# Optimization experiments

Hardware: AMD Instinct MI355X
Metric: run time of the kernel (lower is better)

Reference implementation:

```python
import jax, jax.numpy as jnp
import numpy as np

N, E, FDIM, HID, HEADS, C, L, G = 50000, 800000, 512, 256, 8, 32, 3, 64
EPS = 1e-5


def setup_inputs() -> dict:
    key = jax.random.key(0)
    ks = jax.random.split(key, 16)
    x = jax.random.normal(ks[0], (N, FDIM), dtype=jnp.float32)
    edge_index = jax.random.randint(ks[1], (2, E), 0, N, dtype=jnp.int32)
    batch = jnp.sort(jax.random.randint(ks[2], (N,), 0, G, dtype=jnp.int32))
    s = lambda f: 1.0 / np.sqrt(f)
    return {
        "x": x,
        "edge_index": edge_index,
        "batch": batch,
        "in_w": jax.random.normal(ks[3], (FDIM, HID), jnp.float32) * s(FDIM),
        "in_b": jnp.zeros((HID,), jnp.float32),
        "gat_w": jax.random.normal(ks[4], (L, HID, HID), jnp.float32) * s(HID),
        "att_src": jax.random.normal(ks[5], (L, HEADS, C), jnp.float32) * s(C),
        "att_dst": jax.random.normal(ks[6], (L, HEADS, C), jnp.float32) * s(C),
        "gat_b": jnp.zeros((L, HID), jnp.float32),
        "res_w": jax.random.normal(ks[7], (L, HID, HID), jnp.float32) * s(HID),
        "res_b": jnp.zeros((L, HID), jnp.float32),
        "ln_g": jnp.ones((L, HID), jnp.float32),
        "ln_b": jnp.zeros((L, HID), jnp.float32),
        "pool_w": jax.random.normal(ks[8], (2 * HID, HID), jnp.float32) * s(2 * HID),
        "pool_b": jnp.zeros((HID,), jnp.float32),
    }


def _gat_layer(h, src, dst, w, a_src, a_dst, b):
    # PyG GATConv, concat=True, negative_slope=0.2, dropout inactive (eval)
    xh = (h @ w).reshape(N, HEADS, C)                      # [N,H,C]
    asn = jnp.einsum('nhc,hc->nh', xh, a_src)              # [N,H]
    adn = jnp.einsum('nhc,hc->nh', xh, a_dst)
    e = jax.nn.leaky_relu(asn[src] + adn[dst], 0.2)        # [E2,H]
    # scatter-softmax over destination neighborhoods
    m = jax.ops.segment_max(e, dst, num_segments=N)
    m = jnp.where(jnp.isfinite(m), m, 0.0)
    ex = jnp.exp(e - m[dst])
    den = jax.ops.segment_sum(ex, dst, num_segments=N)
    alpha = ex / (den[dst] + 1e-16)                        # [E2,H]
    msg = xh[src] * alpha[:, :, None]                      # [E2,H,C]
    out = jax.ops.segment_sum(msg, dst, num_segments=N)    # [N,H,C]
    return out.reshape(N, HID) + b


def _layer_norm(h, g, b):
    mu = jnp.mean(h, axis=-1, keepdims=True)
    var = jnp.mean((h - mu) ** 2, axis=-1, keepdims=True)
    return (h - mu) * jax.lax.rsqrt(var + EPS) * g + b


def reference(x, edge_index, batch, in_w, in_b, gat_w, att_src, att_dst, gat_b,
              res_w, res_b, ln_g, ln_b, pool_w, pool_b):
    loops = jnp.arange(N, dtype=edge_index.dtype)          # GATConv add_self_loops=True
    src = jnp.concatenate([edge_index[0], loops])
    dst = jnp.concatenate([edge_index[1], loops])
    h = x @ in_w + in_b
    for i in range(L):
        h_res = h @ res_w[i] + res_b[i]
        h = _gat_layer(h, src, dst, gat_w[i], att_src[i], att_dst[i], gat_b[i])
        h = jax.nn.relu(_layer_norm(h + h_res, ln_g[i], ln_b[i]))
    ones = jnp.ones((N,), h.dtype)
    cnt = jax.ops.segment_sum(ones, batch, num_segments=G)
    h_mean = jax.ops.segment_sum(h, batch, num_segments=G) / jnp.maximum(cnt, 1.0)[:, None]
    h_max = jax.ops.segment_max(h, batch, num_segments=G)
    h_cat = jnp.concatenate([h_mean, h_max], axis=1)       # [G, 2*HID]
    return jax.nn.relu(h_cat @ pool_w + pool_b)            # [G, HID]
```

## Files before the change

kernel.cpp:

```cpp
#include <hip/hip_runtime.h>
#include <math.h>

#define N_NODES 50000
#define E_EDGES 800000
#define E2 (E_EDGES + N_NODES)
#define M_PAD 50048
#define FDIM 512
#define HID 256
#define HEADS 8
#define CDIM 32
#define LAYERS 3
#define GRAPHS 64
#define LN_EPS 1e-5f
#define POOL_P 16

typedef unsigned short ushort_t;
typedef __attribute__((ext_vector_type(8))) short short8v;
typedef __attribute__((ext_vector_type(4))) float f32x4;

__device__ __forceinline__ float bf2f(ushort_t u) {
    union { unsigned int i; float f; } v;
    v.i = ((unsigned int)u) << 16;
    return v.f;
}
__device__ __forceinline__ ushort_t f2bf(float f) {
    union { float f; unsigned int u; } v;
    v.f = f;
    unsigned int r = (v.u + 0x7FFFu + ((v.u >> 16) & 1u)) >> 16;
    return (ushort_t)r;
}
__device__ __forceinline__ void gload_lds16(const void* g, void* l) {
    __builtin_amdgcn_global_load_lds(
        (const __attribute__((address_space(1))) void*)g,
        (__attribute__((address_space(3))) void*)l, 16, 0, 0);
}

__global__ void k_count(const int* __restrict__ ei, int* __restrict__ cnt) {
    int e = blockIdx.x * 256 + threadIdx.x;
    if (e >= E2) return;
    int dst = (e < E_EDGES) ? ei[E_EDGES + e] : (e - E_EDGES);
    atomicAdd(&cnt[dst], 1);
}

__global__ void k_scan1(const int* __restrict__ cnt, int* __restrict__ part) {
    __shared__ int s[256];
    int t = threadIdx.x;
    int i = blockIdx.x * 256 + t;
    s[t] = (i < N_NODES) ? cnt[i] : 0;
    __syncthreads();
    for (int d = 128; d > 0; d >>= 1) {
        if (t < d) s[t] += s[t + d];
        __syncthreads();
    }
    if (t == 0) part[blockIdx.x] = s[0];
}

__global__ void k_scan2(int* __restrict__ part, int nb, int* __restrict__ rowptr) {
    __shared__ int s[256];
    int t = threadIdx.x;
    int v = (t < nb) ? part[t] : 0;
    s[t] = v;
    __syncthreads();
    for (int d = 1; d < 256; d <<= 1) {
        int x = (t >= d) ? s[t - d] : 0;
        __syncthreads();
        s[t] += x;
        __syncthreads();
    }
    if (t < nb) part[t] = s[t] - v;
    if (t == 255) rowptr[N_NODES] = s[255];
}

__global__ void k_scan3(const int* __restrict__ cnt, const int* __restrict__ part,
                        int* __restrict__ rowptr) {
    __shared__ int s[256];
    int t = threadIdx.x;
    int i = blockIdx.x * 256 + t;
    int v = (i < N_NODES) ? cnt[i] : 0;
    s[t] = v;
    __syncthreads();
    for (int d = 1; d < 256; d <<= 1) {
        int x = (t >= d) ? s[t - d] : 0;
        __syncthreads();
        s[t] += x;
        __syncthreads();
    }
    if (i < N_NODES) rowptr[i] = part[blockIdx.x] + s[t] - v;
}

__global__ void k_fill(const int* __restrict__ ei, const int* __restrict__ rowptr,
                       int* __restrict__ fill, int* __restrict__ colv) {
    int e = blockIdx.x * 256 + threadIdx.x;
    if (e >= E2) return;
    int src, dst;
    if (e < E_EDGES) { src = ei[e]; dst = ei[E_EDGES + e]; }
    else             { src = dst = e - E_EDGES; }
    int pos = atomicAdd(&fill[dst], 1);
    colv[rowptr[dst] + pos] = src;
}

__global__ void k_bounds(const int* __restrict__ batch, int* __restrict__ rowstart) {
    int n = blockIdx.x * 256 + threadIdx.x;
    if (n >= N_NODES) return;
    int b = batch[n];
    int bp = (n == 0) ? -1 : batch[n - 1];
    for (int g = bp + 1; g <= b; ++g) rowstart[g] = n;
    if (n == N_NODES - 1) {
        for (int g = b + 1; g <= GRAPHS; ++g) rowstart[g] = N_NODES;
    }
}

__global__ __launch_bounds__(256) void k_cast_x(const float* __restrict__ x,
                                                ushort_t* __restrict__ xb) {
    long long i8 = ((long long)blockIdx.x * 256 + threadIdx.x) * 8;
    if (i8 >= (long long)M_PAD * FDIM) return;
    int row = (int)(i8 >> 9);
    ushort_t o[8];
    if (row < N_NODES) {
        const float* p = x + i8;
        #pragma unroll
        for (int j = 0; j < 8; ++j) o[j] = f2bf(p[j]);
    } else {
        #pragma unroll
        for (int j = 0; j < 8; ++j) o[j] = 0;
    }
    *(short8v*)(xb + i8) = *(short8v*)o;
}

#define IN_ELEMS (FDIM * HID)
#define MAT_ELEMS (HID * HID)
#define WT_TOTAL (IN_ELEMS + 2 * LAYERS * MAT_ELEMS)
__global__ __launch_bounds__(256) void k_wtrans_all(const float* __restrict__ in_w,
                                                    const float* __restrict__ gat_w,
                                                    const float* __restrict__ res_w,
                                                    ushort_t* __restrict__ wt_in,
                                                    ushort_t* __restrict__ wt2) {
    int id = blockIdx.x * 256 + threadIdx.x;
    if (id >= WT_TOTAL) return;
    if (id < IN_ELEMS) {
        int k = id >> 8, n = id & 255;
        wt_in[(size_t)n * FDIM + k] = f2bf(in_w[id]);
    } else {
        int r = id - IN_ELEMS;
        int mat = r >> 16;
        int layer = mat >> 1;
        int isgat = mat & 1;
        int within = r & 65535;
        int k = within >> 8, n = within & 255;
        const float* W = (isgat ? gat_w : res_w) + (size_t)layer * MAT_ELEMS;
        wt2[(size_t)layer * 512 * HID + (size_t)(isgat * 256 + n) * HID + k] =
            f2bf(W[within]);
    }
}

template<int K>
__global__ __launch_bounds__(256) void k_gemm_bf16(const ushort_t* __restrict__ A,
                                                   const ushort_t* __restrict__ BT,
                                                   const float* __restrict__ bias0,
                                                   ushort_t* __restrict__ C0,
                                                   ushort_t* __restrict__ C1,
                                                   const float* __restrict__ a_src,
                                                   const float* __restrict__ a_dst,
                                                   float* __restrict__ asn,
                                                   float* __restrict__ adn, int M) {
    __shared__ char lds[32768] __attribute__((aligned(16)));
    constexpr int NT = K / 32;
    const int bm = blockIdx.x * 128;
    const int bn = blockIdx.y * 128;
    const int t = threadIdx.x, w = t >> 6, l = t & 63;
    const int wr = w >> 1, wc = w & 1;

    const int c1 = t, c2 = t + 256;
    const int ar1 = c1 >> 2, as1 = (c1 & 3) ^ ((ar1 >> 1) & 3);
    const int ar2 = c2 >> 2, as2 = (c2 & 3) ^ ((ar2 >> 1) & 3);
    const ushort_t* pa1 = A + (size_t)(bm + ar1) * K + as1 * 8;
    const ushort_t* pa2 = A + (size_t)(bm + ar2) * K + as2 * 8;
    const ushort_t* pb1 = BT + (size_t)(bn + ar1) * K + as1 * 8;
    const ushort_t* pb2 = BT + (size_t)(bn + ar2) * K + as2 * 8;

    int aoff[4], boff[4];
    const int kb = l >> 4;
    #pragma unroll
    for (int mi = 0; mi < 4; ++mi) {
        int r = wr * 64 + mi * 16 + (l & 15);
        aoff[mi] = r * 64 + ((kb ^ ((r >> 1) & 3)) << 4);
        int c = wc * 64 + mi * 16 + (l & 15);
        boff[mi] = 8192 + c * 64 + ((kb ^ ((c >> 1) & 3)) << 4);
    }

    auto STAGE = [&](int buf, int k0) {
        char* base = lds + buf * 16384;
        gload_lds16(pa1 + k0, base + w * 1024);
        gload_lds16(pa2 + k0, base + 4096 + w * 1024);
        gload_lds16(pb1 + k0, base + 8192 + w * 1024);
        gload_lds16(pb2 + k0, base + 12288 + w * 1024);
    };

    STAGE(0, 0);
    f32x4 acc[4][4] = {};
    #pragma unroll
    for (int tt = 0; tt < NT; ++tt) {
        if (tt + 1 < NT) {
            STAGE((tt + 1) & 1, (tt + 1) * 32);
            asm volatile("s_waitcnt vmcnt(4)" ::: "memory");
        } else {
            asm volatile("s_waitcnt vmcnt(0)" ::: "memory");
        }
        __builtin_amdgcn_s_barrier();
        const char* base = lds + (tt & 1) * 16384;
        short8v a[4], b[4];
        #pragma unroll
        for (int mi = 0; mi < 4; ++mi) a[mi] = *(const short8v*)(base + aoff[mi]);
        #pragma unroll
        for (int ni = 0; ni < 4; ++ni) b[ni] = *(const short8v*)(base + boff[ni]);
        #pragma unroll
        for (int mi = 0; mi < 4; ++mi)
            #pragma unroll
            for (int ni = 0; ni < 4; ++ni)
                acc[mi][ni] = __builtin_amdgcn_mfma_f32_16x16x32_bf16(
                    a[mi], b[ni], acc[mi][ni], 0, 0, 0);
        __builtin_amdgcn_s_barrier();
    }

    ushort_t* C = (bn < 256) ? C0 : C1;
    const float* bias = (bn < 256) ? bias0 : nullptr;
    const int cb = (bn < 256) ? bn : bn - 256;
    #pragma unroll
    for (int mi = 0; mi < 4; ++mi) {
        int row = bm + wr * 64 + mi * 16 + (l >> 4) * 4;
        #pragma unroll
        for (int ni = 0; ni < 4; ++ni) {
            int col = cb + wc * 64 + ni * 16 + (l & 15);
            float bv = bias ? bias[col] : 0.f;
            #pragma unroll
            for (int r = 0; r < 4; ++r) {
                if (row + r < M)
                    C[(size_t)(row + r) * HID + col] = f2bf(acc[mi][ni][r] + bv);
            }
        }
    }

    if (asn && bn >= 256) {
        const int cbase = bn - 256;
        #pragma unroll
        for (int mi = 0; mi < 4; ++mi) {
            int row = bm + wr * 64 + mi * 16 + (l >> 4) * 4;
            #pragma unroll
            for (int p = 0; p < 2; ++p) {
                int c0 = cbase + wc * 64 + (2 * p) * 16 + (l & 15);
                int c1c = c0 + 16;
                int head = c0 >> 5;
                float as0 = a_src[c0], as1 = a_src[c1c];
                float ad0 = a_dst[c0], ad1 = a_dst[c1c];
                float vs[4], vd[4];
                #pragma unroll
                for (int r = 0; r < 4; ++r) {
                    vs[r] = acc[mi][2 * p][r] * as0 + acc[mi][2 * p + 1][r] * as1;
                    vd[r] = acc[mi][2 * p][r] * ad0 + acc[mi][2 * p + 1][r] * ad1;
                }
                #pragma unroll
                for (int d = 1; d < 16; d <<= 1) {
                    #pragma unroll
                    for (int r = 0; r < 4; ++r) {
                        vs[r] += __shfl_xor(vs[r], d);
                        vd[r] += __shfl_xor(vd[r], d);
                    }
                }
                if ((l & 15) == 0) {
                    #pragma unroll
                    for (int r = 0; r < 4; ++r) {
                        if (row + r < N_NODES) {
                            asn[(row + r) * HEADS + head] = vs[r];
                            adn[(row + r) * HEADS + head] = vd[r];
                        }
                    }
                }
            }
        }
    }
}

__global__ __launch_bounds__(256) void k_agg_ln(const ushort_t* __restrict__ xhb,
                                                const float* __restrict__ asn,
                                                const float* __restrict__ adn,
                                                const int* __restrict__ rowptr,
                                                const int* __restrict__ colv,
                                                const ushort_t* __restrict__ hresb,
                                                const float* __restrict__ gb,
                                                const float* __restrict__ g,
                                                const float* __restrict__ b,
                                                ushort_t* __restrict__ hb) {
    const int wave = threadIdx.x >> 6, lane = threadIdx.x & 63;
    const int n = blockIdx.x * 4 + wave;
    if (n >= N_NODES) return;
    const int half = lane >> 5;
    const int lh = lane & 31;
    const int head = lh >> 2;
    const int ch0 = lh * 8;
    const float adn_h = adn[n * HEADS + head];
    const int j0 = rowptr[n], j1 = rowptr[n + 1];

    float acc[8] = {};
    float den = 0.f;
    int base = j0;
    for (; base + 8 <= j1; base += 8) {
        int idx[4];
        #pragma unroll
        for (int q = 0; q < 4; ++q) idx[q] = colv[base + 2 * q + half];
        short8v u[4];
        #pragma unroll
        for (int q = 0; q < 4; ++q)
            u[q] = *(const short8v*)(xhb + (size_t)idx[q] * HID + ch0);
        float p[4];
        #pragma unroll
        for (int q = 0; q < 4; ++q) {
            float e = asn[idx[q] * HEADS + head] + adn_h;
            e = (e > 0.f) ? e : 0.2f * e;
            p[q] = __expf(e);
        }
        #pragma unroll
        for (int q = 0; q < 4; ++q) {
            den += p[q];
            #pragma unroll
            for (int c = 0; c < 8; ++c)
                acc[c] += p[q] * bf2f((ushort_t)u[q][c]);
        }
    }
    for (; base < j1; base += 2) {
        bool valid = (base + half) < j1;
        int s = valid ? colv[base + half] : n;
        short8v u = *(const short8v*)(xhb + (size_t)s * HID + ch0);
        float e = asn[s * HEADS + head] + adn_h;
        e = (e > 0.f) ? e : 0.2f * e;
        float p = valid ? __expf(e) : 0.f;
        den += p;
        #pragma unroll
        for (int c = 0; c < 8; ++c)
            acc[c] += p * bf2f((ushort_t)u[c]);
    }
    den += __shfl_xor(den, 32);
    #pragma unroll
    for (int c = 0; c < 8; ++c) acc[c] += __shfl_xor(acc[c], 32);

    const float inv = 1.f / (den + 1e-16f);
    short8v hr = *(const short8v*)(hresb + (size_t)n * HID + ch0);
    float4 gbA = *(const float4*)(gb + ch0);
    float4 gbB = *(const float4*)(gb + ch0 + 4);
    float v[8];
    #pragma unroll
    for (int c = 0; c < 8; ++c) {
        float gbv = (c < 4) ? ((const float*)&gbA)[c] : ((const float*)&gbB)[c - 4];
        v[c] = acc[c] * inv + bf2f((ushort_t)hr[c]) + gbv;
    }
    float s = 0.f;
    #pragma unroll
    for (int c = 0; c < 8; ++c) s += v[c];
    #pragma unroll
    for (int d = 1; d < 32; d <<= 1) s += __shfl_xor(s, d);
    const float mu = s * (1.f / HID);
    float q = 0.f;
    #pragma unroll
    for (int c = 0; c < 8; ++c) {
        v[c] -= mu;
        q += v[c] * v[c];
    }
    #pragma unroll
    for (int d = 1; d < 32; d <<= 1) q += __shfl_xor(q, d);
    const float rstd = rsqrtf(q * (1.f / HID) + LN_EPS);
    float4 gA = *(const float4*)(g + ch0);
    float4 gB = *(const float4*)(g + ch0 + 4);
    float4 bA = *(const float4*)(b + ch0);
    float4 bB = *(const float4*)(b + ch0 + 4);
    ushort_t o[8];
    #pragma unroll
    for (int c = 0; c < 8; ++c) {
        float gv = (c < 4) ? ((const float*)&gA)[c] : ((const float*)&gB)[c - 4];
        float bv = (c < 4) ? ((const float*)&bA)[c] : ((const float*)&bB)[c - 4];
        o[c] = f2bf(fmaxf(v[c] * rstd * gv + bv, 0.f));
    }
    if (half == 0)
        *(short8v*)(hb + (size_t)n * HID + ch0) = *(short8v*)o;
}

__global__ __launch_bounds__(256) void k_pool1(const ushort_t* __restrict__ hb,
                                               const int* __restrict__ rowstart,
                                               float* __restrict__ part) {
    int g = blockIdx.x, p = blockIdx.y, c = threadIdx.x;
    int s0 = rowstart[g], s1 = rowstart[g + 1];
    float sum = 0.f, mx = -INFINITY;
    for (int n = s0 + p; n < s1; n += POOL_P) {
        float v = bf2f(hb[(size_t)n * HID + c]);
        sum += v;
        mx = fmaxf(mx, v);
    }
    float* pp = part + (size_t)(g * POOL_P + p) * 512;
    pp[c] = sum;
    pp[256 + c] = mx;
}

__global__ __launch_bounds__(256) void k_pool2g(const float* __restrict__ part,
                                                const int* __restrict__ rowstart,
                                                const float* __restrict__ W,
                                                const float* __restrict__ bias,
                                                float* __restrict__ out) {
    __shared__ float hc[512];
    int g = blockIdx.x, c = threadIdx.x;
    float sum = 0.f, mx = -INFINITY;
    for (int p = 0; p < POOL_P; ++p) {
        const float* pp = part + (size_t)(g * POOL_P + p) * 512;
        sum += pp[c];
        mx = fmaxf(mx, pp[256 + c]);
    }
    float cntf = (float)(rowstart[g + 1] - rowstart[g]);
    hc[c] = sum / fmaxf(cntf, 1.f);
    hc[256 + c] = mx;
    __syncthreads();
    float acc = bias[c];
    #pragma unroll 8
    for (int k = 0; k < 2 * HID; ++k)
        acc += hc[k] * W[(size_t)k * HID + c];
    out[(size_t)g * HID + c] = fmaxf(acc, 0.f);
}

extern "C" void kernel_launch(void* const* d_in, const int* in_sizes, int n_in,
                              void* d_out, int out_size, void* d_ws, size_t ws_size,
                              hipStream_t stream) {
    const float* x       = (const float*)d_in[0];
    const int*   ei      = (const int*)d_in[1];
    const int*   batch   = (const int*)d_in[2];
    const float* in_w    = (const float*)d_in[3];
    const float* in_b    = (const float*)d_in[4];
    const float* gat_w   = (const float*)d_in[5];
    const float* att_src = (const float*)d_in[6];
    const float* att_dst = (const float*)d_in[7];
    const float* gat_b   = (const float*)d_in[8];
    const float* res_w   = (const float*)d_in[9];
    const float* res_b   = (const float*)d_in[10];
    const float* ln_g    = (const float*)d_in[11];
    const float* ln_b    = (const float*)d_in[12];
    const float* pool_w  = (const float*)d_in[13];
    const float* pool_b  = (const float*)d_in[14];
    float* out = (float*)d_out;

    char* ws = (char*)d_ws;
    size_t off = 0;
    auto alloc = [&](size_t bytes) -> char* {
        char* p = ws + off;
        off = (off + bytes + 255) & ~(size_t)255;
        return p;
    };
    ushort_t* xb    = (ushort_t*)alloc((size_t)M_PAD * FDIM * 2);
    ushort_t* hb    = (ushort_t*)alloc((size_t)M_PAD * HID * 2);
    ushort_t* xhb   = (ushort_t*)alloc((size_t)M_PAD * HID * 2);
    ushort_t* hresb = (ushort_t*)alloc((size_t)M_PAD * HID * 2);
    float* asn      = (float*)alloc((size_t)N_NODES * HEADS * 4);
    float* adn      = (float*)alloc((size_t)N_NODES * HEADS * 4);
    int*   cnt      = (int*)alloc((size_t)N_NODES * 4);
    int*   fill     = (int*)alloc((size_t)N_NODES * 4);
    int*   rowptr   = (int*)alloc((size_t)(N_NODES + 1) * 4);
    int*   colv     = (int*)alloc((size_t)E2 * 4);
    int*   part     = (int*)alloc(256 * 4);
    int*   rowstart = (int*)alloc((size_t)(GRAPHS + 1) * 4);
    ushort_t* wt_in = (ushort_t*)alloc((size_t)HID * FDIM * 2);
    ushort_t* wt2   = (ushort_t*)alloc((size_t)LAYERS * 512 * HID * 2);
    float* poolpart = (float*)alloc((size_t)GRAPHS * POOL_P * 512 * 4);

    hipMemsetAsync(cnt, 0, (size_t)N_NODES * 4, stream);
    hipMemsetAsync(fill, 0, (size_t)N_NODES * 4, stream);

    const int ge = (E2 + 255) / 256;
    const int nb = (N_NODES + 255) / 256;
    k_count<<<ge, 256, 0, stream>>>(ei, cnt);
    k_scan1<<<nb, 256, 0, stream>>>(cnt, part);
    k_scan2<<<1, 256, 0, stream>>>(part, nb, rowptr);
    k_scan3<<<nb, 256, 0, stream>>>(cnt, part, rowptr);
    k_fill<<<ge, 256, 0, stream>>>(ei, rowptr, fill, colv);
    k_bounds<<<nb, 256, 0, stream>>>(batch, rowstart);

    k_cast_x<<<(int)(((size_t)M_PAD * FDIM / 8 + 255) / 256), 256, 0, stream>>>(x, xb);
    k_wtrans_all<<<(WT_TOTAL + 255) / 256, 256, 0, stream>>>(in_w, gat_w, res_w,
                                                             wt_in, wt2);

    dim3 gg1(M_PAD / 128, 2);
    k_gemm_bf16<FDIM><<<gg1, 256, 0, stream>>>(xb, wt_in, in_b, hb, nullptr,
                                               nullptr, nullptr, nullptr, nullptr,
                                               N_NODES);

    const int nw = (N_NODES + 3) / 4;
    dim3 gg2(M_PAD / 128, 4);
    for (int i = 0; i < LAYERS; ++i) {
        k_gemm_bf16<HID><<<gg2, 256, 0, stream>>>(hb, wt2 + (size_t)i * 512 * HID,
                                                  res_b + (size_t)i * HID,
                                                  hresb, xhb,
                                                  att_src + (size_t)i * HEADS * CDIM,
                                                  att_dst + (size_t)i * HEADS * CDIM,
                                                  asn, adn, N_NODES);
        k_agg_ln<<<nw, 256, 0, stream>>>(xhb, asn, adn, rowptr, colv, hresb,
                                         gat_b + (size_t)i * HID,
                                         ln_g + (size_t)i * HID,
                                         ln_b + (size_t)i * HID, hb);
    }
    dim3 pg(GRAPHS, POOL_P);
    k_pool1<<<pg, 256, 0, stream>>>(hb, rowstart, poolpart);
    k_pool2g<<<GRAPHS, 256, 0, stream>>>(poolpart, rowstart, pool_w, pool_b, out);
}
```

Measured before the change: 625.4 us.

## Use K=64 single-buffered GEMM tiles and N-fastest block order

The bf16 GEMM now stages 64-wide K slices into one 32KB LDS buffer with an 8-way XOR swizzle, replacing the double-buffered 32-wide slices. Each slice feeds two MFMA sub-steps, which halves the number of barrier rounds. The grid is also transposed so that blocks sharing the same A rows run next to each other, which should improve L2 reuse of A. In exchange, global loads no longer overlap with compute inside a block, so the kernel relies on other resident blocks to hide memory latency.

```diff
diff --git a/kernel.cpp b/kernel.cpp
--- a/kernel.cpp
+++ b/kernel.cpp
@@ -164,62 +164,60 @@
                                                    float* __restrict__ asn,
                                                    float* __restrict__ adn, int M) {
     __shared__ char lds[32768] __attribute__((aligned(16)));
-    constexpr int NT = K / 32;
-    const int bm = blockIdx.x * 128;
-    const int bn = blockIdx.y * 128;
+    constexpr int NT = K / 64;
+    const int bn = blockIdx.x * 128;
+    const int bm = blockIdx.y * 128;
     const int t = threadIdx.x, w = t >> 6, l = t & 63;
     const int wr = w >> 1, wc = w & 1;
 
-    const int c1 = t, c2 = t + 256;
-    const int ar1 = c1 >> 2, as1 = (c1 & 3) ^ ((ar1 >> 1) & 3);
-    const int ar2 = c2 >> 2, as2 = (c2 & 3) ^ ((ar2 >> 1) & 3);
-    const ushort_t* pa1 = A + (size_t)(bm + ar1) * K + as1 * 8;
-    const ushort_t* pa2 = A + (size_t)(bm + ar2) * K + as2 * 8;
-    const ushort_t* pb1 = BT + (size_t)(bn + ar1) * K + as1 * 8;
-    const ushort_t* pb2 = BT + (size_t)(bn + ar2) * K + as2 * 8;
-
-    int aoff[4], boff[4];
+    const int trow = t >> 3;
+    const int slotl = (t & 7) ^ (trow & 7);
+    const ushort_t* pa[4];
+    const ushort_t* pb[4];
+    #pragma unroll
+    for (int i = 0; i < 4; ++i) {
+        pa[i] = A + (size_t)(bm + i * 32 + trow) * K + slotl * 8;
+        pb[i] = BT + (size_t)(bn + i * 32 + trow) * K + slotl * 8;
+    }
+    const int dst0 = t * 16;
+
+    int aoff[4][2], boff[4][2];
     const int kb = l >> 4;
     #pragma unroll
     for (int mi = 0; mi < 4; ++mi) {
         int r = wr * 64 + mi * 16 + (l & 15);
-        aoff[mi] = r * 64 + ((kb ^ ((r >> 1) & 3)) << 4);
         int c = wc * 64 + mi * 16 + (l & 15);
-        boff[mi] = 8192 + c * 64 + ((kb ^ ((c >> 1) & 3)) << 4);
-    }
-
-    auto STAGE = [&](int buf, int k0) {
-        char* base = lds + buf * 16384;
-        gload_lds16(pa1 + k0, base + w * 1024);
-        gload_lds16(pa2 + k0, base + 4096 + w * 1024);
-        gload_lds16(pb1 + k0, base + 8192 + w * 1024);
-        gload_lds16(pb2 + k0, base + 12288 + w * 1024);
-    };
-
-    STAGE(0, 0);
+        #pragma unroll
+        for (int ks = 0; ks < 2; ++ks) {
+            aoff[mi][ks] = r * 128 + (((ks * 4 + kb) ^ (r & 7)) << 4);
+            boff[mi][ks] = 16384 + c * 128 + (((ks * 4 + kb) ^ (c & 7)) << 4);
+        }
+    }
+
     f32x4 acc[4][4] = {};
-    #pragma unroll
     for (int tt = 0; tt < NT; ++tt) {
-        if (tt + 1 < NT) {
-            STAGE((tt + 1) & 1, (tt + 1) * 32);
-            asm volatile("s_waitcnt vmcnt(4)" ::: "memory");
-        } else {
-            asm volatile("s_waitcnt vmcnt(0)" ::: "memory");
-        }
-        __builtin_amdgcn_s_barrier();
-        const char* base = lds + (tt & 1) * 16384;
-        short8v a[4], b[4];
-        #pragma unroll
-        for (int mi = 0; mi < 4; ++mi) a[mi] = *(const short8v*)(base + aoff[mi]);
-        #pragma unroll
-        for (int ni = 0; ni < 4; ++ni) b[ni] = *(const short8v*)(base + boff[ni]);
-        #pragma unroll
-        for (int mi = 0; mi < 4; ++mi)
+        const int k0 = tt * 64;
+        #pragma unroll
+        for (int i = 0; i < 4; ++i) {
+            gload_lds16(pa[i] + k0, lds + i * 4096 + dst0);
+            gload_lds16(pb[i] + k0, lds + 16384 + i * 4096 + dst0);
+        }
+        __syncthreads();
+        #pragma unroll
+        for (int ks = 0; ks < 2; ++ks) {
+            short8v a[4], b[4];
             #pragma unroll
-            for (int ni = 0; ni < 4; ++ni)
-                acc[mi][ni] = __builtin_amdgcn_mfma_f32_16x16x32_bf16(
-                    a[mi], b[ni], acc[mi][ni], 0, 0, 0);
-        __builtin_amdgcn_s_barrier();
+            for (int mi = 0; mi < 4; ++mi) a[mi] = *(const short8v*)(lds + aoff[mi][ks]);
+            #pragma unroll
+            for (int ni = 0; ni < 4; ++ni) b[ni] = *(const short8v*)(lds + boff[ni][ks]);
+            #pragma unroll
+            for (int mi = 0; mi < 4; ++mi)
+                #pragma unroll
+                for (int ni = 0; ni < 4; ++ni)
+                    acc[mi][ni] = __builtin_amdgcn_mfma_f32_16x16x32_bf16(
+                        a[mi], b[ni], acc[mi][ni], 0, 0, 0);
+        }
+        __syncthreads();
     }
 
     ushort_t* C = (bn < 256) ? C0 : C1;
@@ -481,13 +479,13 @@
     k_wtrans_all<<<(WT_TOTAL + 255) / 256, 256, 0, stream>>>(in_w, gat_w, res_w,
                                                              wt_in, wt2);
 
-    dim3 gg1(M_PAD / 128, 2);
+    dim3 gg1(2, M_PAD / 128);
     k_gemm_bf16<FDIM><<<gg1, 256, 0, stream>>>(xb, wt_in, in_b, hb, nullptr,
                                                nullptr, nullptr, nullptr, nullptr,
                                                N_NODES);
 
     const int nw = (N_NODES + 3) / 4;
-    dim3 gg2(M_PAD / 128, 4);
+    dim3 gg2(4, M_PAD / 128);
     for (int i = 0; i < LAYERS; ++i) {
         k_gemm_bf16<HID><<<gg2, 256, 0, stream>>>(hb, wt2 + (size_t)i * 512 * HID,
                                                   res_b + (size_t)i * HID,
```

Result: slower. 654.5 us (+4.7%).

## Fold input projection into first layer weights and drop GEMM double buffering

Applied to the files above, without the earlier changes.

Precomputes combined weights in_w·[res_w0|gat_w0] and matching biases, so the input projection and the first layer's GEMM become one K=512 GEMM writing hres and xh directly. This removes a full N×256 GEMM pass and its intermediate write and read of h. Separately, the GEMM main loop drops the double-buffered LDS pipeline for a single buffer with full syncs, which halves LDS use but exposes global load latency. Rounding changes slightly because the combined weights are cast to bf16 once.

```diff
diff --git a/kernel.cpp b/kernel.cpp
--- a/kernel.cpp
+++ b/kernel.cpp
@@ -129,42 +129,73 @@
 
 #define IN_ELEMS (FDIM * HID)
 #define MAT_ELEMS (HID * HID)
-#define WT_TOTAL (IN_ELEMS + 2 * LAYERS * MAT_ELEMS)
-__global__ __launch_bounds__(256) void k_wtrans_all(const float* __restrict__ in_w,
-                                                    const float* __restrict__ gat_w,
+#define WT_TOTAL (2 * LAYERS * MAT_ELEMS)
+__global__ __launch_bounds__(256) void k_wtrans_all(const float* __restrict__ gat_w,
                                                     const float* __restrict__ res_w,
-                                                    ushort_t* __restrict__ wt_in,
                                                     ushort_t* __restrict__ wt2) {
-    int id = blockIdx.x * 256 + threadIdx.x;
-    if (id >= WT_TOTAL) return;
-    if (id < IN_ELEMS) {
-        int k = id >> 8, n = id & 255;
-        wt_in[(size_t)n * FDIM + k] = f2bf(in_w[id]);
-    } else {
-        int r = id - IN_ELEMS;
-        int mat = r >> 16;
-        int layer = mat >> 1;
-        int isgat = mat & 1;
-        int within = r & 65535;
-        int k = within >> 8, n = within & 255;
-        const float* W = (isgat ? gat_w : res_w) + (size_t)layer * MAT_ELEMS;
-        wt2[(size_t)layer * 512 * HID + (size_t)(isgat * 256 + n) * HID + k] =
-            f2bf(W[within]);
-    }
+    int r = blockIdx.x * 256 + threadIdx.x;
+    if (r >= WT_TOTAL) return;
+    int mat = r >> 16;
+    int layer = mat >> 1;
+    int isgat = mat & 1;
+    int within = r & 65535;
+    int k = within >> 8, n = within & 255;
+    const float* W = (isgat ? gat_w : res_w) + (size_t)layer * MAT_ELEMS;
+    wt2[(size_t)layer * 512 * HID + (size_t)(isgat * 256 + n) * HID + k] =
+        f2bf(W[within]);
+}
+
+__global__ __launch_bounds__(256) void k_wcomb(const float* __restrict__ in_w,
+                                               const ushort_t* __restrict__ wt2_0,
+                                               ushort_t* __restrict__ wtC) {
+    __shared__ float wrow[HID];
+    int n = blockIdx.x;
+    wrow[threadIdx.x] = bf2f(wt2_0[(size_t)n * HID + threadIdx.x]);
+    __syncthreads();
+    #pragma unroll
+    for (int h = 0; h < 2; ++h) {
+        int f = h * 256 + threadIdx.x;
+        const float* irow = in_w + (size_t)f * HID;
+        float s = 0.f;
+        #pragma unroll 4
+        for (int k = 0; k < HID; k += 4) {
+            float4 iv = *(const float4*)(irow + k);
+            s += iv.x * wrow[k] + iv.y * wrow[k + 1]
+               + iv.z * wrow[k + 2] + iv.w * wrow[k + 3];
+        }
+        wtC[(size_t)n * FDIM + f] = f2bf(s);
+    }
+}
+
+__global__ __launch_bounds__(256) void k_bcomb(const float* __restrict__ in_b,
+                                               const float* __restrict__ res_w0,
+                                               const float* __restrict__ gat_w0,
+                                               const float* __restrict__ res_b0,
+                                               float* __restrict__ bC0,
+                                               float* __restrict__ bC1) {
+    int n = threadIdx.x;
+    float s0 = 0.f, s1 = 0.f;
+    for (int k = 0; k < HID; ++k) {
+        float ib = in_b[k];
+        s0 += ib * res_w0[(size_t)k * HID + n];
+        s1 += ib * gat_w0[(size_t)k * HID + n];
+    }
+    bC0[n] = s0 + res_b0[n];
+    bC1[n] = s1;
 }
 
 template<int K>
 __global__ __launch_bounds__(256) void k_gemm_bf16(const ushort_t* __restrict__ A,
                                                    const ushort_t* __restrict__ BT,
                                                    const float* __restrict__ bias0,
+                                                   const float* __restrict__ bias1,
                                                    ushort_t* __restrict__ C0,
                                                    ushort_t* __restrict__ C1,
                                                    const float* __restrict__ a_src,
                                                    const float* __restrict__ a_dst,
                                                    float* __restrict__ asn,
                                                    float* __restrict__ adn, int M) {
-    __shared__ char lds[32768] __attribute__((aligned(16)));
-    constexpr int NT = K / 32;
+    __shared__ char lds[16384] __attribute__((aligned(16)));
     const int bm = blockIdx.x * 128;
     const int bn = blockIdx.y * 128;
     const int t = threadIdx.x, w = t >> 6, l = t & 63;
@@ -177,6 +208,10 @@
     const ushort_t* pa2 = A + (size_t)(bm + ar2) * K + as2 * 8;
     const ushort_t* pb1 = BT + (size_t)(bn + ar1) * K + as1 * 8;
     const ushort_t* pb2 = BT + (size_t)(bn + ar2) * K + as2 * 8;
+    char* la1 = lds + w * 1024;
+    char* la2 = lds + 4096 + w * 1024;
+    char* lb1 = lds + 8192 + w * 1024;
+    char* lb2 = lds + 12288 + w * 1024;
 
     int aoff[4], boff[4];
     const int kb = l >> 4;
@@ -188,42 +223,29 @@
         boff[mi] = 8192 + c * 64 + ((kb ^ ((c >> 1) & 3)) << 4);
     }
 
-    auto STAGE = [&](int buf, int k0) {
-        char* base = lds + buf * 16384;
-        gload_lds16(pa1 + k0, base + w * 1024);
-        gload_lds16(pa2 + k0, base + 4096 + w * 1024);
-        gload_lds16(pb1 + k0, base + 8192 + w * 1024);
-        gload_lds16(pb2 + k0, base + 12288 + w * 1024);
-    };
-
-    STAGE(0, 0);
     f32x4 acc[4][4] = {};
-    #pragma unroll
-    for (int tt = 0; tt < NT; ++tt) {
-        if (tt + 1 < NT) {
-            STAGE((tt + 1) & 1, (tt + 1) * 32);
-            asm volatile("s_waitcnt vmcnt(4)" ::: "memory");
-        } else {
-            asm volatile("s_waitcnt vmcnt(0)" ::: "memory");
-        }
-        __builtin_amdgcn_s_barrier();
-        const char* base = lds + (tt & 1) * 16384;
+    for (int k0 = 0; k0 < K; k0 += 32) {
+        gload_lds16(pa1 + k0, la1);
+        gload_lds16(pa2 + k0, la2);
+        gload_lds16(pb1 + k0, lb1);
+        gload_lds16(pb2 + k0, lb2);
+        __syncthreads();
         short8v a[4], b[4];
         #pragma unroll
-        for (int mi = 0; mi < 4; ++mi) a[mi] = *(const short8v*)(base + aoff[mi]);
-        #pragma unroll
-        for (int ni = 0; ni < 4; ++ni) b[ni] = *(const short8v*)(base + boff[ni]);
+        for (int mi = 0; mi < 4; ++mi) a[mi] = *(const short8v*)(lds + aoff[mi]);
+        #pragma unroll
+        for (int ni = 0; ni < 4; ++ni) b[ni] = *(const short8v*)(lds + boff[ni]);
         #pragma unroll
         for (int mi = 0; mi < 4; ++mi)
             #pragma unroll
             for (int ni = 0; ni < 4; ++ni)
                 acc[mi][ni] = __builtin_amdgcn_mfma_f32_16x16x32_bf16(
                     a[mi], b[ni], acc[mi][ni], 0, 0, 0);
-        __builtin_amdgcn_s_barrier();
+        __syncthreads();
     }
 
     ushort_t* C = (bn < 256) ? C0 : C1;
-    const float* bias = (bn < 256) ? bias0 : nullptr;
+    const float* bias = (bn < 256) ? bias0 : bias1;
     const int cb = (bn < 256) ? bn : bn - 256;
     #pragma unroll
     for (int mi = 0; mi < 4; ++mi) {
@@ -250,13 +272,17 @@
                 int c0 = cbase + wc * 64 + (2 * p) * 16 + (l & 15);
                 int c1c = c0 + 16;
                 int head = c0 >> 5;
+                float b1a = bias1 ? bias1[c0] : 0.f;
+                float b1b = bias1 ? bias1[c1c] : 0.f;
                 float as0 = a_src[c0], as1 = a_src[c1c];
                 float ad0 = a_dst[c0], ad1 = a_dst[c1c];
                 float vs[4], vd[4];
                 #pragma unroll
                 for (int r = 0; r < 4; ++r) {
-                    vs[r] = acc[mi][2 * p][r] * as0 + acc[mi][2 * p + 1][r] * as1;
-                    vd[r] = acc[mi][2 * p][r] * ad0 + acc[mi][2 * p + 1][r] * ad1;
+                    float x0 = acc[mi][2 * p][r] + b1a;
+                    float x1 = acc[mi][2 * p + 1][r] + b1b;
+                    vs[r] = x0 * as0 + x1 * as1;
+                    vd[r] = x0 * ad0 + x1 * ad1;
                 }
                 #pragma unroll
                 for (int d = 1; d < 16; d <<= 1) {
@@ -461,8 +487,10 @@
     int*   colv     = (int*)alloc((size_t)E2 * 4);
     int*   part     = (int*)alloc(256 * 4);
     int*   rowstart = (int*)alloc((size_t)(GRAPHS + 1) * 4);
-    ushort_t* wt_in = (ushort_t*)alloc((size_t)HID * FDIM * 2);
     ushort_t* wt2   = (ushort_t*)alloc((size_t)LAYERS * 512 * HID * 2);
+    ushort_t* wtC   = (ushort_t*)alloc((size_t)512 * FDIM * 2);
+    float* bC0      = (float*)alloc(HID * 4);
+    float* bC1      = (float*)alloc(HID * 4);
     float* poolpart = (float*)alloc((size_t)GRAPHS * POOL_P * 512 * 4);
 
     hipMemsetAsync(cnt, 0, (size_t)N_NODES * 4, stream);
@@ -478,23 +506,25 @@
     k_bounds<<<nb, 256, 0, stream>>>(batch, rowstart);
 
     k_cast_x<<<(int)(((size_t)M_PAD * FDIM / 8 + 255) / 256), 256, 0, stream>>>(x, xb);
-    k_wtrans_all<<<(WT_TOTAL + 255) / 256, 256, 0, stream>>>(in_w, gat_w, res_w,
-                                                             wt_in, wt2);
-
-    dim3 gg1(M_PAD / 128, 2);
-    k_gemm_bf16<FDIM><<<gg1, 256, 0, stream>>>(xb, wt_in, in_b, hb, nullptr,
-                                               nullptr, nullptr, nullptr, nullptr,
-                                               N_NODES);
+    k_wtrans_all<<<(WT_TOTAL + 255) / 256, 256, 0, stream>>>(gat_w, res_w, wt2);
+    k_wcomb<<<512, 256, 0, stream>>>(in_w, wt2, wtC);
+    k_bcomb<<<1, 256, 0, stream>>>(in_b, res_w, gat_w, res_b, bC0, bC1);
 
     const int nw = (N_NODES + 3) / 4;
-    dim3 gg2(M_PAD / 128, 4);
-    for (int i = 0; i < LAYERS; ++i) {
-        k_gemm_bf16<HID><<<gg2, 256, 0, stream>>>(hb, wt2 + (size_t)i * 512 * HID,
-                                                  res_b + (size_t)i * HID,
-                                                  hresb, xhb,
-                                                  att_src + (size_t)i * HEADS * CDIM,
-                                                  att_dst + (size_t)i * HEADS * CDIM,
-                                                  asn, adn, N_NODES);
+    dim3 gg(M_PAD / 128, 4);
+
+    k_gemm_bf16<FDIM><<<gg, 256, 0, stream>>>(xb, wtC, bC0, bC1, hresb, xhb,
+                                              att_src, att_dst, asn, adn, N_NODES);
+    k_agg_ln<<<nw, 256, 0, stream>>>(xhb, asn, adn, rowptr, colv, hresb,
+                                     gat_b, ln_g, ln_b, hb);
+
+    for (int i = 1; i < LAYERS; ++i) {
+        k_gemm_bf16<HID><<<gg, 256, 0, stream>>>(hb, wt2 + (size_t)i * 512 * HID,
+                                                 res_b + (size_t)i * HID, nullptr,
+                                                 hresb, xhb,
+                                                 att_src + (size_t)i * HEADS * CDIM,
+                                                 att_dst + (size_t)i * HEADS * CDIM,
+                                                 asn, adn, N_NODES);
         k_agg_ln<<<nw, 256, 0, stream>>>(xhb, asn, adn, rowptr, colv, hresb,
                                          gat_b + (size_t)i * HID,
                                          ln_g + (size_t)i * HID,
```

New measurement: 652.3 us. 4.3% more time.
